# Optimization experiments

Hardware: AMD Instinct MI355X
Metric: run time of the kernel (lower is better)

Reference implementation:

```python
import jax, jax.numpy as jnp
import numpy as np

B, N, D = 2, 8192, 1024
H, DH = 8, 64  # heads, dim_head; inner = H*DH = 512
INNER = H * DH


def setup_inputs() -> dict:
    key = jax.random.key(0)
    k1, k2, k3 = jax.random.split(key, 3)
    x = jax.random.normal(k1, (B, N, D), dtype=jnp.float32)
    # xavier_uniform-ish scaling for weights
    W_qkv = jax.random.normal(k2, (D, 3 * INNER), dtype=jnp.float32) * (1.0 / np.sqrt(D))
    W_out = jax.random.normal(k3, (INNER, D), dtype=jnp.float32) * (1.0 / np.sqrt(INNER))
    b_out = jnp.zeros((D,), dtype=jnp.float32)
    return {"x": x, "W_qkv": W_qkv, "W_out": W_out, "b_out": b_out}


def reference(x, W_qkv, W_out, b_out):
    b, n, d = x.shape
    qkv = x @ W_qkv                               # [b, n, 3*inner]
    q, k, v = jnp.split(qkv, 3, axis=-1)          # each [b, n, inner]

    def to_heads(t):
        return t.reshape(b, n, H, DH).transpose(0, 2, 1, 3)  # [b, h, n, dh]

    q, k, v = to_heads(q), to_heads(k), to_heads(v)
    q = jax.nn.softmax(q, axis=-1)                # over dim_head
    k = jax.nn.softmax(k, axis=-2)                # over sequence
    # context: k^T v  -> [b, h, dh, dh]
    context = jnp.einsum('bhnd,bhne->bhde', k, v)
    out = jnp.einsum('bhnd,bhde->bhne', q, context)  # [b, h, n, dh]
    out = out.transpose(0, 2, 1, 3).reshape(b, n, INNER)
    return out @ W_out + b_out                    # [b, n, d]
```

## Files before the change

### kernel.cpp

```cpp
#include <hip/hip_runtime.h>
#include <stdint.h>


typedef _Float16 half4 __attribute__((ext_vector_type(4)));
typedef _Float16 half8 __attribute__((ext_vector_type(8)));
typedef float f32x4 __attribute__((ext_vector_type(4)));

#define WS_XB 0UL
#define WS_WQKVT 33554432UL
#define WS_CWT 37748736UL
#define WS_CTXPART 54525952UL
#define WS_COLPART 71303168UL
#define WS_SQ 88080384UL

__device__ __forceinline__ void gld16(const void* g, void* l) {
  __builtin_amdgcn_global_load_lds(
      (const __attribute__((address_space(1))) unsigned int*)g,
      (__attribute__((address_space(3))) unsigned int*)l, 16, 0, 0);
}

__global__ void prep_kernel(const float* __restrict__ x,
                            const float* __restrict__ Wqkv,
                            _Float16* __restrict__ xb,
                            _Float16* __restrict__ wqkvT) {
  const int blk = blockIdx.x;
  if (blk < 16384) {
    int i = blk * 256 + threadIdx.x;
    f32x4 v = *(const f32x4*)(x + (size_t)i * 4);
    half4 h = {(_Float16)v[0], (_Float16)v[1], (_Float16)v[2], (_Float16)v[3]};
    *(half4*)(xb + (size_t)i * 4) = h;
  } else {
    int i = (blk - 16384) * 256 + threadIdx.x;
    int c = i >> 10, r = i & 1023;
    wqkvT[i] = (_Float16)Wqkv[(size_t)r * 1536 + c];
  }
}


__device__ __forceinline__ void stage_tile(const _Float16* __restrict__ G, int K,
                                           int rowbase, int kt, char* region,
                                           int t) {
  char* wbase = region + (t & ~63) * 16;
#pragma unroll
  for (int q = 0; q < 4; ++q) {
    const int row = q * 32 + (t >> 3);
    const int col8 = ((t & 7) ^ (row & 7)) * 8;
    gld16(G + (size_t)(rowbase + row) * K + kt + col8, wbase + q * 4096);
  }
}

__device__ __forceinline__ void stage_tile64(const _Float16* __restrict__ G,
                                             int K, int rowbase, int kt,
                                             char* region, int t) {
  char* wbase = region + (t & ~63) * 16;
#pragma unroll
  for (int q = 0; q < 2; ++q) {
    const int row = q * 32 + (t >> 3);
    const int col8 = ((t & 7) ^ (row & 7)) * 8;
    gld16(G + (size_t)(rowbase + row) * K + kt + col8, wbase + q * 4096);
  }
}

template <int EPI>
__global__ __launch_bounds__(256, 2) void gemm128(
    const _Float16* __restrict__ A, const _Float16* __restrict__ BT, int K,
    int NTN, int bstride, _Float16* __restrict__ oQ,
    float* __restrict__ ctxpart, float* __restrict__ colpart,
    float* __restrict__ oC, const float* __restrict__ bias) {
  __shared__ char lds[65536];
  const int t = threadIdx.x;
  const int l = t & 63, w = t >> 6;
  const int wm = w >> 1, wn = w & 1;
  const int fr = l & 15, qq = l >> 4;
  const int swzx = (fr & 7) << 4;

  const int nwg = gridDim.x;
  const int cpx = nwg >> 3;
  const int wg = (blockIdx.x & 7) * cpx + (blockIdx.x >> 3);
  const int tileM = wg / NTN, tileN = wg - tileM * NTN;
  const int mbase = tileM * 128, nbase = tileN * 128;
  BT += (size_t)(tileM >> 6) * bstride;

  const int NT = K >> 6;
  f32x4 acc[4][4] = {};
  half8 a[4][2], b[4][2];

  auto STG = [&](int tile) {
    int kt = tile * 64;
    if (kt > K - 64) kt = K - 64;
    char* base = lds + ((tile & 1) << 15);
    stage_tile(A, K, mbase, kt, base, t);
    if (EPI == 1 || tileN < 4) {
      stage_tile(BT, K, nbase, kt, base + 16384, t);
    } else {
      const int h = tileN - 4;
      stage_tile64(BT, K, 512 + h * 64, kt, base + 16384, t);
      stage_tile64(BT, K, 1024 + h * 64, kt, base + 16384 + 8192, t);
    }
  };

  STG(0);
  STG(1);
  asm volatile("s_waitcnt vmcnt(8)" ::: "memory");
  __builtin_amdgcn_s_barrier();

  for (int t2 = 0; t2 < NT; ++t2) {
    const char* ldsA = lds + ((t2 & 1) << 15);
    const char* ldsB = ldsA + 16384;
    STG(t2 + 1);
#pragma unroll
    for (int mi = 0; mi < 4; ++mi)
#pragma unroll
      for (int kk = 0; kk < 2; ++kk) {
        int off = (wm * 64 + mi * 16 + fr) * 128 + ((kk * 64 + qq * 16) ^ swzx);
        a[mi][kk] = *(const half8*)(ldsA + off);
      }
#pragma unroll
    for (int ni = 0; ni < 4; ++ni)
#pragma unroll
      for (int kk = 0; kk < 2; ++kk) {
        int off = (wn * 64 + ni * 16 + fr) * 128 + ((kk * 64 + qq * 16) ^ swzx);
        b[ni][kk] = *(const half8*)(ldsB + off);
      }
    __builtin_amdgcn_s_barrier();
    __builtin_amdgcn_s_setprio(1);
#pragma unroll
    for (int mi = 0; mi < 4; ++mi)
#pragma unroll
      for (int ni = 0; ni < 2; ++ni)
#pragma unroll
        for (int kk = 0; kk < 2; ++kk)
          acc[mi][ni] = __builtin_amdgcn_mfma_f32_16x16x32_f16(
              a[mi][kk], b[ni][kk], acc[mi][ni], 0, 0, 0);
    __builtin_amdgcn_s_setprio(0);
    asm volatile("s_waitcnt vmcnt(0) lgkmcnt(0)" ::: "memory");
    __builtin_amdgcn_s_barrier();
    __builtin_amdgcn_s_setprio(1);
#pragma unroll
    for (int mi = 0; mi < 4; ++mi)
#pragma unroll
      for (int ni = 2; ni < 4; ++ni)
#pragma unroll
        for (int kk = 0; kk < 2; ++kk)
          acc[mi][ni] = __builtin_amdgcn_mfma_f32_16x16x32_f16(
              a[mi][kk], b[ni][kk], acc[mi][ni], 0, 0, 0);
    __builtin_amdgcn_s_setprio(0);
  }

  if (EPI == 0) {
    if (tileN < 4) {
      const int gcol0 = nbase + wn * 64;
#pragma unroll
      for (int mi = 0; mi < 4; ++mi) {
        const int grow = mbase + wm * 64 + mi * 16 + qq * 4;
        float e[4][4], rs[4];
#pragma unroll
        for (int r = 0; r < 4; ++r) {
          float s = 0.f;
#pragma unroll
          for (int ni = 0; ni < 4; ++ni) {
            e[ni][r] = __expf(acc[mi][ni][r]);
            s += e[ni][r];
          }
#pragma unroll
          for (int off = 1; off < 16; off <<= 1) s += __shfl_xor(s, off, 64);
          rs[r] = 1.f / s;
        }
#pragma unroll
        for (int ni = 0; ni < 4; ++ni) {
          const int gcol = gcol0 + ni * 16 + fr;
#pragma unroll
          for (int r = 0; r < 4; ++r)
            oQ[(size_t)(grow + r) * 512 + gcol] = (_Float16)(e[ni][r] * rs[r]);
        }
      }
    } else {
      const int h = tileN - 4;
      float* credu = (float*)(lds + 32768);
      if (wn == 0) {
#pragma unroll
        for (int mi = 0; mi < 4; ++mi)
#pragma unroll
          for (int ni = 0; ni < 4; ++ni) {
            f32x4 e4;
#pragma unroll
            for (int r = 0; r < 4; ++r) e4[r] = __expf(acc[mi][ni][r]);
            acc[mi][ni] = e4;
          }
        float s[4] = {};
#pragma unroll
        for (int ni = 0; ni < 4; ++ni) {
#pragma unroll
          for (int mi = 0; mi < 4; ++mi)
#pragma unroll
            for (int r = 0; r < 4; ++r) s[ni] += acc[mi][ni][r];
          s[ni] += __shfl_xor(s[ni], 16, 64);
          s[ni] += __shfl_xor(s[ni], 32, 64);
        }
        if (l < 16) {
#pragma unroll
          for (int ni = 0; ni < 4; ++ni) credu[wm * 64 + ni * 16 + fr] = s[ni];
        }
      }
      {
        char* dst8 = lds + (wn ? 16384 : 0);
#pragma unroll
        for (int mi = 0; mi < 4; ++mi) {
          const int nb = (wm * 64 + mi * 16 + qq * 4) * 2;
#pragma unroll
          for (int ni = 0; ni < 4; ++ni) {
            const int c = ni * 16 + fr;
            half4 pk = {(_Float16)acc[mi][ni][0], (_Float16)acc[mi][ni][1],
                        (_Float16)acc[mi][ni][2], (_Float16)acc[mi][ni][3]};
            *(half4*)(dst8 + c * 256 + (nb ^ ((c & 15) << 4))) = pk;
          }
        }
      }
      __syncthreads();
      half8 bf[4];
      const int erow = w * 16 + fr;
#pragma unroll
      for (int kk = 0; kk < 4; ++kk)
        bf[kk] = *(const half8*)(lds + 16384 + erow * 256 +
                                 ((kk * 64 + qq * 16) ^ ((erow & 15) << 4)));
      f32x4 dacc[4] = {};
#pragma unroll
      for (int mi = 0; mi < 4; ++mi) {
        const int drow = mi * 16 + fr;
#pragma unroll
        for (int kk = 0; kk < 4; ++kk) {
          half8 af = *(const half8*)(lds + drow * 256 +
                                     ((kk * 64 + qq * 16) ^ ((drow & 15) << 4)));
          dacc[mi] =
              __builtin_amdgcn_mfma_f32_16x16x32_f16(af, bf[kk], dacc[mi], 0, 0, 0);
        }
      }
      const int bh = (tileM >> 6) * 8 + h, chunk = tileM & 63;
      float* cp = ctxpart + ((size_t)bh * 64 + chunk) * 4096;
#pragma unroll
      for (int mi = 0; mi < 4; ++mi)
#pragma unroll
        for (int r = 0; r < 4; ++r)
          cp[(mi * 16 + qq * 4 + r) * 64 + w * 16 + fr] = dacc[mi][r];
      if (t < 16) {
        f32x4 c0 = *(const f32x4*)&credu[t * 4];
        f32x4 c1 = *(const f32x4*)&credu[64 + t * 4];
        *(f32x4*)&colpart[((size_t)bh * 64 + chunk) * 64 + t * 4] = c0 + c1;
      }
    }
  } else {
#pragma unroll
    for (int mi = 0; mi < 4; ++mi) {
      const int grow = mbase + wm * 64 + mi * 16 + qq * 4;
#pragma unroll
      for (int ni = 0; ni < 4; ++ni) {
        const int gcol = nbase + wn * 64 + ni * 16 + fr;
        const float bb = bias[gcol];
#pragma unroll
        for (int r = 0; r < 4; ++r)
          oC[(size_t)(grow + r) * 1024 + gcol] = acc[mi][ni][r] + bb;
      }
    }
  }
}

__global__ __launch_bounds__(256) void ctxw_kernel(
    const float* __restrict__ ctxpart, const float* __restrict__ colpart,
    const float* __restrict__ Wout, _Float16* __restrict__ cwT) {
  __shared__ float part[4][64];
  __shared__ float csp[64];
  __shared__ float crow[64];
  const int blk = blockIdx.x;
  const int bh = blk >> 6, d = blk & 63;
  const int b = bh >> 3, h = bh & 7;
  const int t = threadIdx.x;
  const int e = t & 63, cq = t >> 6;
  float p = 0.f;
#pragma unroll
  for (int cc = 0; cc < 16; ++cc)
    p += ctxpart[((size_t)bh * 64 + cq * 16 + cc) * 4096 + d * 64 + e];
  part[cq][e] = p;
  if (t >= 64 && t < 128)
    csp[t - 64] = colpart[((size_t)bh * 64 + (t - 64)) * 64 + d];
  __syncthreads();
  if (t < 64) {
    float csum = 0.f;
#pragma unroll
    for (int c = 0; c < 64; ++c) csum += csp[c];
    crow[t] = (part[0][t] + part[1][t] + part[2][t] + part[3][t]) / csum;
  }
  __syncthreads();
  float acc[4] = {};
  for (int e2 = 0; e2 < 64; ++e2) {
    const float c = crow[e2];
    const float* wr = Wout + (size_t)(h * 64 + e2) * 1024 + t;
#pragma unroll
    for (int j = 0; j < 4; ++j) acc[j] += c * wr[j * 256];
  }
  _Float16* dst = cwT + (size_t)b * 524288 + (size_t)t * 512 + h * 64 + d;
#pragma unroll
  for (int j = 0; j < 4; ++j) dst[(size_t)j * 256 * 512] = (_Float16)acc[j];
}

extern "C" void kernel_launch(void* const* d_in, const int* in_sizes, int n_in,
                              void* d_out, int out_size, void* d_ws, size_t ws_size,
                              hipStream_t stream) {
  const float* x = (const float*)d_in[0];
  const float* Wqkv = (const float*)d_in[1];
  const float* Wout = (const float*)d_in[2];
  const float* bout = (const float*)d_in[3];
  float* out = (float*)d_out;
  char* ws = (char*)d_ws;

  _Float16* xb = (_Float16*)(ws + WS_XB);
  _Float16* wqkvT = (_Float16*)(ws + WS_WQKVT);
  _Float16* cwT = (_Float16*)(ws + WS_CWT);
  _Float16* sq = (_Float16*)(ws + WS_SQ);
  float* ctxpart = (float*)(ws + WS_CTXPART);
  float* colpart = (float*)(ws + WS_COLPART);

  prep_kernel<<<22528, 256, 0, stream>>>(x, Wqkv, xb, wqkvT);
  gemm128<0><<<1536, 256, 0, stream>>>(xb, wqkvT, 1024, 12, 0, sq, ctxpart,
                                       colpart, nullptr, nullptr);
  ctxw_kernel<<<1024, 256, 0, stream>>>(ctxpart, colpart, Wout, cwT);
  gemm128<1><<<1024, 256, 0, stream>>>(sq, cwT, 512, 8, 524288, nullptr,
                                       nullptr, nullptr, out, bout);
}
```

Baseline: 135.9 us.

## Tile the weight transpose through LDS and store context partials in fp16

The weight transpose in prep_kernel now goes through a padded 64x64 LDS tile. This gives vectorized, coalesced reads and writes in place of the strided scalar gather, and cuts the transpose grid from 6144 blocks to 384. The per-chunk context partials that gemm128 writes and ctxw_kernel reads are now stored as fp16 instead of fp32, halving that intermediate traffic. The cost is lower precision in the partial sums before the fp32 reduction, which could slightly change the accuracy of the normalized context.

```diff
diff --git a/kernel.cpp b/kernel.cpp
--- a/kernel.cpp
+++ b/kernel.cpp
@@ -24,15 +24,33 @@
                             _Float16* __restrict__ xb,
                             _Float16* __restrict__ wqkvT) {
   const int blk = blockIdx.x;
+  const int t = threadIdx.x;
   if (blk < 16384) {
-    int i = blk * 256 + threadIdx.x;
+    int i = blk * 256 + t;
     f32x4 v = *(const f32x4*)(x + (size_t)i * 4);
     half4 h = {(_Float16)v[0], (_Float16)v[1], (_Float16)v[2], (_Float16)v[3]};
     *(half4*)(xb + (size_t)i * 4) = h;
   } else {
-    int i = (blk - 16384) * 256 + threadIdx.x;
-    int c = i >> 10, r = i & 1023;
-    wqkvT[i] = (_Float16)Wqkv[(size_t)r * 1536 + c];
+    __shared__ float sT[64 * 65];
+    const int tb = blk - 16384;
+    const int r0 = (tb & 15) * 64, c0 = (tb >> 4) * 64;
+    const int lr = t >> 4, lc4 = (t & 15) * 4;
+#pragma unroll
+    for (int s = 0; s < 4; ++s) {
+      const int row = s * 16 + lr;
+      f32x4 v = *(const f32x4*)&Wqkv[(size_t)(r0 + row) * 1536 + c0 + lc4];
+#pragma unroll
+      for (int j = 0; j < 4; ++j) sT[(lc4 + j) * 65 + row] = v[j];
+    }
+    __syncthreads();
+#pragma unroll
+    for (int s = 0; s < 4; ++s) {
+      const int cl = s * 16 + lr;
+      half4 o = {(_Float16)sT[cl * 65 + lc4], (_Float16)sT[cl * 65 + lc4 + 1],
+                 (_Float16)sT[cl * 65 + lc4 + 2],
+                 (_Float16)sT[cl * 65 + lc4 + 3]};
+      *(half4*)&wqkvT[(size_t)(c0 + cl) * 1024 + r0 + lc4] = o;
+    }
   }
 }
 
@@ -65,7 +83,7 @@
 __global__ __launch_bounds__(256, 2) void gemm128(
     const _Float16* __restrict__ A, const _Float16* __restrict__ BT, int K,
     int NTN, int bstride, _Float16* __restrict__ oQ,
-    float* __restrict__ ctxpart, float* __restrict__ colpart,
+    _Float16* __restrict__ ctxpart, float* __restrict__ colpart,
     float* __restrict__ oC, const float* __restrict__ bias) {
   __shared__ char lds[65536];
   const int t = threadIdx.x;
@@ -236,12 +254,13 @@
         }
       }
       const int bh = (tileM >> 6) * 8 + h, chunk = tileM & 63;
-      float* cp = ctxpart + ((size_t)bh * 64 + chunk) * 4096;
+      _Float16* cp = ctxpart + ((size_t)bh * 64 + chunk) * 4096;
 #pragma unroll
       for (int mi = 0; mi < 4; ++mi)
 #pragma unroll
         for (int r = 0; r < 4; ++r)
-          cp[(mi * 16 + qq * 4 + r) * 64 + w * 16 + fr] = dacc[mi][r];
+          cp[(mi * 16 + qq * 4 + r) * 64 + w * 16 + fr] =
+              (_Float16)dacc[mi][r];
       if (t < 16) {
         f32x4 c0 = *(const f32x4*)&credu[t * 4];
         f32x4 c1 = *(const f32x4*)&credu[64 + t * 4];
@@ -265,7 +284,7 @@
 }
 
 __global__ __launch_bounds__(256) void ctxw_kernel(
-    const float* __restrict__ ctxpart, const float* __restrict__ colpart,
+    const _Float16* __restrict__ ctxpart, const float* __restrict__ colpart,
     const float* __restrict__ Wout, _Float16* __restrict__ cwT) {
   __shared__ float part[4][64];
   __shared__ float csp[64];
@@ -278,7 +297,7 @@
   float p = 0.f;
 #pragma unroll
   for (int cc = 0; cc < 16; ++cc)
-    p += ctxpart[((size_t)bh * 64 + cq * 16 + cc) * 4096 + d * 64 + e];
+    p += (float)ctxpart[((size_t)bh * 64 + cq * 16 + cc) * 4096 + d * 64 + e];
   part[cq][e] = p;
   if (t >= 64 && t < 128)
     csp[t - 64] = colpart[((size_t)bh * 64 + (t - 64)) * 64 + d];
@@ -316,10 +335,10 @@
   _Float16* wqkvT = (_Float16*)(ws + WS_WQKVT);
   _Float16* cwT = (_Float16*)(ws + WS_CWT);
   _Float16* sq = (_Float16*)(ws + WS_SQ);
-  float* ctxpart = (float*)(ws + WS_CTXPART);
+  _Float16* ctxpart = (_Float16*)(ws + WS_CTXPART);
   float* colpart = (float*)(ws + WS_COLPART);
 
-  prep_kernel<<<22528, 256, 0, stream>>>(x, Wqkv, xb, wqkvT);
+  prep_kernel<<<16768, 256, 0, stream>>>(x, Wqkv, xb, wqkvT);
   gemm128<0><<<1536, 256, 0, stream>>>(xb, wqkvT, 1024, 12, 0, sq, ctxpart,
                                        colpart, nullptr, nullptr);
   ctxw_kernel<<<1024, 256, 0, stream>>>(ctxpart, colpart, Wout, cwT);
```

New measurement: 131.2 us, median of 2. 1.04x faster.
